# Kernel optimization log

Hardware: AMD Instinct MI355X
Metric: run time of the kernel (lower is better)

## Reference

```python
import jax, jax.numpy as jnp
import numpy as np

N_PAIR = 32
N_ENTI = 36          # VidVRD object classes (+pad)
N_CLS_TOT = 133      # 132 predicate classes + background id 0
NUM_BASE = 92        # split='base' -> pids 1..92
N_CTX = 8
MAX_L = 40           # GeneralAlproCfg.max_txt_len
D = 768


def setup_inputs() -> dict:
    key = jax.random.key(0)
    ks = jax.random.split(key, 11)
    std = 0.02
    return {
        "so_cls_ids": jax.random.randint(ks[0], (N_PAIR, 2), 0, N_ENTI, dtype=jnp.int64),
        "enti_txt_embds": jax.random.normal(ks[1], (N_ENTI, 256), jnp.float32),
        "prefix_embds": jax.random.normal(ks[2], (N_CLS_TOT, 1, D), jnp.float32) * std,
        "suffix_embds": jax.random.normal(ks[3], (N_CLS_TOT, MAX_L - 1 - N_CTX, D), jnp.float32) * std,
        "token_mask": jnp.ones((N_CLS_TOT, MAX_L), jnp.int32),
        "meta_ctx_embds": jax.random.normal(ks[4], (N_CTX, D), jnp.float32) * std,
        "subj_ctx_embds": jax.random.normal(ks[5], (N_CTX, D), jnp.float32) * std,
        "obj_ctx_embds": jax.random.normal(ks[6], (N_CTX, D), jnp.float32) * std,
        "W1": jax.random.normal(ks[7], (512, 256), jnp.float32) * std,
        "b1": jnp.zeros((256,), jnp.float32),
        "W2": jax.random.normal(ks[8], (256, 2 * D), jnp.float32) * std,
    }


def reference(so_cls_ids, enti_txt_embds, prefix_embds, suffix_embds, token_mask,
              meta_ctx_embds, subj_ctx_embds, obj_ctx_embds, W1, b1, W2):
    n_pair = so_cls_ids.shape[0]
    pids = jnp.arange(1, NUM_BASE + 1)                      # split='base'
    n_cls = NUM_BASE

    # entity text-embedding gather + tiny MLP
    s_embd = enti_txt_embds[so_cls_ids[:, 0]]               # [n_pair, 256]
    o_embd = enti_txt_embds[so_cls_ids[:, 1]]
    so = jnp.concatenate([s_embd, o_embd], axis=-1)         # [n_pair, 512]
    h = jax.nn.relu(so @ W1 + b1)                           # [n_pair, 256]
    so_e = h @ W2                                           # [n_pair, 1536]
    s_q, o_q = so_e[:, :D], so_e[:, D:]

    # softmax attention over meta context (keys = values = meta_ctx_embds)
    scale = 1.0 / jnp.sqrt(jnp.asarray(D, jnp.float32))
    s_att = jax.nn.softmax(s_q @ meta_ctx_embds.T * scale, axis=-1) @ meta_ctx_embds  # [n_pair, D]
    o_att = jax.nn.softmax(o_q @ meta_ctx_embds.T * scale, axis=-1) @ meta_ctx_embds

    s_ctx = subj_ctx_embds[None, :, :] + s_att[:, None, :]  # [n_pair, n_ctx, D]
    o_ctx = obj_ctx_embds[None, :, :] + o_att[:, None, :]

    prefix = prefix_embds[pids]                             # [n_cls, 1, D]
    suffix = suffix_embds[pids]                             # [n_cls, L_suf, D]
    l_suf = suffix.shape[1]

    def build(ctx):
        return jnp.concatenate([
            jnp.broadcast_to(prefix[None], (n_pair, n_cls, 1, D)),
            jnp.broadcast_to(ctx[:, None], (n_pair, n_cls, N_CTX, D)),
            jnp.broadcast_to(suffix[None], (n_pair, n_cls, l_suf, D)),
        ], axis=2).reshape(n_pair * n_cls, MAX_L, D)

    subj_token_embds = build(s_ctx)                         # [n_pair*n_cls, MAX_L, D]
    obj_token_embds = build(o_ctx)
    mask = jnp.tile(token_mask[pids], (n_pair, 1))          # [n_pair*n_cls, MAX_L]
    return subj_token_embds, obj_token_embds, mask
```

## Files before the change

### kernel.cpp

```cpp
#include <hip/hip_runtime.h>
#include <hip/hip_bf16.h>

typedef unsigned int u32;
typedef __attribute__((ext_vector_type(4))) float f32x4;

#define NPAIR 32
#define NCLS  92
#define NCTX  8
#define MAXL  40
#define DIM   768
#define LSUF  31

#define MAT_ELEMS 90439680u
#define MASK_BASE 180879360u
#define NBLK_D1   1472u
#define MASK_F4   29440u
#define NBLK_MASK 115u

#define WS_ATT  0u
#define WS_H    49152u
#define WS_SOE  57344u

__global__ __launch_bounds__(512) void k_h(
    const int* __restrict__ so_ids,
    const float* __restrict__ enti,
    const float* __restrict__ W1,
    const float* __restrict__ b1,
    float* __restrict__ ws)
{
    const int p = blockIdx.x;
    const int t = threadIdx.x;
    __shared__ float so_vec[512];
    __shared__ float w1part[2][256];
    __shared__ int ids[2];

    if (t == 0) {
        bool is64 = true;
        for (int i = 1; i < 64; i += 2) is64 = is64 && (so_ids[i] == 0);
        if (is64) { ids[0] = so_ids[4 * p];     ids[1] = so_ids[4 * p + 2]; }
        else      { ids[0] = so_ids[2 * p];     ids[1] = so_ids[2 * p + 1]; }
    }
    __syncthreads();
    so_vec[t] = (t < 256) ? enti[ids[0] * 256 + t] : enti[ids[1] * 256 + (t - 256)];
    __syncthreads();

    const int j = t & 255, half = t >> 8;
    const float* w = W1 + (half * 256) * 256 + j;
    const float* sv = so_vec + half * 256;
    float acc = 0.f;
    #pragma unroll 8
    for (int kk = 0; kk < 256; ++kk)
        acc = fmaf(sv[kk], w[(size_t)kk * 256], acc);
    w1part[half][j] = acc;
    __syncthreads();
    if (t < 256)
        ws[WS_H + p * 256 + t] = fmaxf(w1part[0][t] + w1part[1][t] + b1[t], 0.f);
}

__global__ __launch_bounds__(256) void k_soe(
    const float* __restrict__ W2,
    float* __restrict__ ws)
{
    const int p = blockIdx.x / 6;
    const int cc = blockIdx.x % 6;
    const int t = threadIdx.x;
    __shared__ float hl[256];
    hl[t] = ws[WS_H + p * 256 + t];
    __syncthreads();

    const int c = cc * 256 + t;
    const float* w = W2 + c;
    float acc = 0.f;
    #pragma unroll 8
    for (int k = 0; k < 256; ++k)
        acc = fmaf(hl[k], w[(size_t)k * 1536], acc);
    ws[WS_SOE + p * 1536 + c] = acc;
}

__global__ __launch_bounds__(256) void k_att(
    const float* __restrict__ meta,
    float* __restrict__ ws)
{
    const int which = blockIdx.x >> 5;
    const int p = blockIdx.x & 31;
    const int t = threadIdx.x;
    __shared__ float red[8][256];
    __shared__ float probs[8];

    const float* q = ws + WS_SOE + p * 1536 + which * DIM;
    float qr[3];
    #pragma unroll
    for (int i = 0; i < 3; ++i) qr[i] = q[t + 256 * i];

    #pragma unroll
    for (int c = 0; c < 8; ++c) {
        float pp = 0.f;
        #pragma unroll
        for (int i = 0; i < 3; ++i)
            pp = fmaf(qr[i], meta[c * DIM + t + 256 * i], pp);
        red[c][t] = pp;
    }
    __syncthreads();
    for (int s = 128; s > 0; s >>= 1) {
        if (t < s) {
            #pragma unroll
            for (int c = 0; c < 8; ++c)
                red[c][t] += red[c][t + s];
        }
        __syncthreads();
    }
    if (t == 0) {
        const float scale = 0.036084391824351615f;
        float sc[8], m = -1e30f;
        #pragma unroll
        for (int c = 0; c < 8; ++c) { sc[c] = red[c][0] * scale; m = fmaxf(m, sc[c]); }
        float sum = 0.f;
        #pragma unroll
        for (int c = 0; c < 8; ++c) { sc[c] = expf(sc[c] - m); sum += sc[c]; }
        const float inv = 1.f / sum;
        #pragma unroll
        for (int c = 0; c < 8; ++c) probs[c] = sc[c] * inv;
    }
    __syncthreads();
    #pragma unroll
    for (int i = 0; i < 3; ++i) {
        const int d = t + 256 * i;
        float a = 0.f;
        #pragma unroll
        for (int c = 0; c < 8; ++c)
            a = fmaf(probs[c], meta[c * DIM + d], a);
        ws[WS_ATT + (which * NPAIR + p) * DIM + d] = a;
    }
}

__global__ __launch_bounds__(256) void k_copy(
    const float* __restrict__ prefix,
    const float* __restrict__ suffix,
    const int* __restrict__ tok_mask,
    float* __restrict__ out)
{
    const u32 bid = blockIdx.x;
    const u32 t = threadIdx.x;

    if (bid < NBLK_D1) {
        const u32 which = bid / (NCLS * 8u);
        const u32 rem = bid - which * (NCLS * 8u);
        const u32 cls = rem / 8u;
        const u32 tq = rem - cls * 8u;

        __shared__ __align__(16) float srcl[4 * DIM];
        for (u32 u = t; u < 4u * 192u; u += 256u) {
            const u32 j = u / 192u;
            const u32 dpos = u - j * 192u;
            const u32 rtok = (tq == 0u) ? (j == 0u ? 0u : 8u + j) : (8u + 4u * tq + j);
            const float* src = (rtok == 0u)
                ? (prefix + (size_t)(cls + 1u) * DIM + dpos * 4u)
                : (suffix + ((size_t)(cls + 1u) * LSUF + (rtok - 9u)) * DIM + dpos * 4u);
            *(f32x4*)(srcl + u * 4u) = *(const f32x4*)src;
        }
        __syncthreads();

        for (u32 pair = 0; pair < NPAIR; ++pair) {
            float* slab = out + (size_t)which * MAT_ELEMS
                              + ((size_t)(pair * NCLS + cls) * MAXL) * DIM;
            #pragma unroll
            for (u32 uu = 0; uu < 3u; ++uu) {
                const u32 u = uu * 256u + t;
                const u32 j = u / 192u;
                const u32 dpos = u - j * 192u;
                const u32 rtok = (tq == 0u) ? (j == 0u ? 0u : 8u + j) : (8u + 4u * tq + j);
                __builtin_nontemporal_store(*(const f32x4*)(srcl + u * 4u),
                    (f32x4*)(slab + (size_t)rtok * DIM + dpos * 4u));
            }
        }
    } else {
        const u32 idx4 = (bid - NBLK_D1) * 256u + t;
        if (idx4 < MASK_F4) {
            const u32 m = idx4 * 4u;
            f32x4 v;
            #pragma unroll
            for (int j = 0; j < 4; ++j) {
                const u32 i = m + (u32)j;
                const u32 rw = i / 40u;
                const u32 tk = i - rw * 40u;
                const u32 cls = rw % 92u;
                v[j] = (float)tok_mask[(cls + 1u) * 40u + tk];
            }
            __builtin_nontemporal_store(v, (f32x4*)(out + MASK_BASE + m));
        }
    }
}

__global__ __launch_bounds__(256) void k_ctx(
    const float* __restrict__ sctx,
    const float* __restrict__ octx,
    const float* __restrict__ att,
    float* __restrict__ out)
{
    const u32 bid = blockIdx.x;
    const u32 t = threadIdx.x;
    const u32 which = bid / 128u;
    const u32 rem = bid - which * 128u;
    const u32 pair = rem / 4u;
    const u32 cg = rem & 3u;

    const float* ctx = which ? octx : sctx;
    const float* ar = att + (size_t)(which * NPAIR + pair) * DIM;

    __shared__ __align__(16) float sums[8 * DIM];
    for (u32 u = t; u < 8u * 192u; u += 256u) {
        const u32 dpos = u % 192u;
        const f32x4 v = *(const f32x4*)(ctx + (size_t)u * 4u)
                      + *(const f32x4*)(ar + (size_t)dpos * 4u);
        *(f32x4*)(sums + u * 4u) = v;
    }
    __syncthreads();

    for (u32 c = 0; c < 23u; ++c) {
        const u32 cls = cg * 23u + c;
        float* base = out + (size_t)which * MAT_ELEMS
                          + ((size_t)(pair * NCLS + cls) * MAXL + 1u) * DIM;
        #pragma unroll
        for (u32 uu = 0; uu < 6u; ++uu) {
            const u32 u = uu * 256u + t;
            __builtin_nontemporal_store(*(const f32x4*)(sums + u * 4u),
                (f32x4*)(base + (size_t)u * 4u));
        }
    }
}

extern "C" void kernel_launch(void* const* d_in, const int* in_sizes, int n_in,
                              void* d_out, int out_size, void* d_ws, size_t ws_size,
                              hipStream_t stream) {
    const int* so_ids     = (const int*)d_in[0];
    const float* enti     = (const float*)d_in[1];
    const float* prefix   = (const float*)d_in[2];
    const float* suffix   = (const float*)d_in[3];
    const int* tok_mask   = (const int*)d_in[4];
    const float* meta     = (const float*)d_in[5];
    const float* sctx     = (const float*)d_in[6];
    const float* octx     = (const float*)d_in[7];
    const float* W1       = (const float*)d_in[8];
    const float* b1       = (const float*)d_in[9];
    const float* W2       = (const float*)d_in[10];
    float* ws = (float*)d_ws;

    k_h  <<<dim3(NPAIR), dim3(512), 0, stream>>>(so_ids, enti, W1, b1, ws);
    k_soe<<<dim3(192),   dim3(256), 0, stream>>>(W2, ws);
    k_att<<<dim3(64),    dim3(256), 0, stream>>>(meta, ws);
    k_ctx<<<dim3(256),   dim3(256), 0, stream>>>(sctx, octx, ws + WS_ATT, (float*)d_out);
    k_copy<<<dim3(NBLK_D1 + NBLK_MASK), dim3(256), 0, stream>>>(
        prefix, suffix, tok_mask, (float*)d_out);
}
```

Measured before the change: 171.0 us.

## Fuse MLP, attention, context broadcast and copy kernels into one launch

Merges the five kernels into a single launch. The first 64 blocks each redundantly compute the per-pair MLP, softmax attention and context sum in shared memory, then write context rows for all 92 classes. The remaining blocks do the prefix/suffix broadcast and the mask, unchanged. This removes four launches and the workspace round-trips. In exchange, the 64 context blocks each recompute the W1/W2 matvecs serially, so they may become a long tail, and these blocks are not overlapped with any earlier compute.

Measured after the change: 156.4 us. 8.6% less time.

```diff
diff --git a/kernel.cpp b/kernel.cpp
--- a/kernel.cpp
+++ b/kernel.cpp
@@ -13,142 +13,157 @@
 
 #define MAT_ELEMS 90439680u
 #define MASK_BASE 180879360u
+
+#define NBLK_CTX  64u
 #define NBLK_D1   1472u
-#define MASK_F4   29440u
 #define NBLK_MASK 115u
-
-#define WS_ATT  0u
-#define WS_H    49152u
-#define WS_SOE  57344u
-
-__global__ __launch_bounds__(512) void k_h(
+#define NBLK_ALL  (NBLK_CTX + NBLK_D1 + NBLK_MASK)
+
+__global__ __launch_bounds__(256) void k_fused(
     const int* __restrict__ so_ids,
     const float* __restrict__ enti,
-    const float* __restrict__ W1,
-    const float* __restrict__ b1,
-    float* __restrict__ ws)
-{
-    const int p = blockIdx.x;
-    const int t = threadIdx.x;
-    __shared__ float so_vec[512];
-    __shared__ float w1part[2][256];
-    __shared__ int ids[2];
-
-    if (t == 0) {
-        bool is64 = true;
-        for (int i = 1; i < 64; i += 2) is64 = is64 && (so_ids[i] == 0);
-        if (is64) { ids[0] = so_ids[4 * p];     ids[1] = so_ids[4 * p + 2]; }
-        else      { ids[0] = so_ids[2 * p];     ids[1] = so_ids[2 * p + 1]; }
-    }
-    __syncthreads();
-    so_vec[t] = (t < 256) ? enti[ids[0] * 256 + t] : enti[ids[1] * 256 + (t - 256)];
-    __syncthreads();
-
-    const int j = t & 255, half = t >> 8;
-    const float* w = W1 + (half * 256) * 256 + j;
-    const float* sv = so_vec + half * 256;
-    float acc = 0.f;
-    #pragma unroll 8
-    for (int kk = 0; kk < 256; ++kk)
-        acc = fmaf(sv[kk], w[(size_t)kk * 256], acc);
-    w1part[half][j] = acc;
-    __syncthreads();
-    if (t < 256)
-        ws[WS_H + p * 256 + t] = fmaxf(w1part[0][t] + w1part[1][t] + b1[t], 0.f);
-}
-
-__global__ __launch_bounds__(256) void k_soe(
-    const float* __restrict__ W2,
-    float* __restrict__ ws)
-{
-    const int p = blockIdx.x / 6;
-    const int cc = blockIdx.x % 6;
-    const int t = threadIdx.x;
-    __shared__ float hl[256];
-    hl[t] = ws[WS_H + p * 256 + t];
-    __syncthreads();
-
-    const int c = cc * 256 + t;
-    const float* w = W2 + c;
-    float acc = 0.f;
-    #pragma unroll 8
-    for (int k = 0; k < 256; ++k)
-        acc = fmaf(hl[k], w[(size_t)k * 1536], acc);
-    ws[WS_SOE + p * 1536 + c] = acc;
-}
-
-__global__ __launch_bounds__(256) void k_att(
-    const float* __restrict__ meta,
-    float* __restrict__ ws)
-{
-    const int which = blockIdx.x >> 5;
-    const int p = blockIdx.x & 31;
-    const int t = threadIdx.x;
-    __shared__ float red[8][256];
-    __shared__ float probs[8];
-
-    const float* q = ws + WS_SOE + p * 1536 + which * DIM;
-    float qr[3];
-    #pragma unroll
-    for (int i = 0; i < 3; ++i) qr[i] = q[t + 256 * i];
-
-    #pragma unroll
-    for (int c = 0; c < 8; ++c) {
-        float pp = 0.f;
-        #pragma unroll
-        for (int i = 0; i < 3; ++i)
-            pp = fmaf(qr[i], meta[c * DIM + t + 256 * i], pp);
-        red[c][t] = pp;
-    }
-    __syncthreads();
-    for (int s = 128; s > 0; s >>= 1) {
-        if (t < s) {
-            #pragma unroll
-            for (int c = 0; c < 8; ++c)
-                red[c][t] += red[c][t + s];
-        }
-        __syncthreads();
-    }
-    if (t == 0) {
-        const float scale = 0.036084391824351615f;
-        float sc[8], m = -1e30f;
-        #pragma unroll
-        for (int c = 0; c < 8; ++c) { sc[c] = red[c][0] * scale; m = fmaxf(m, sc[c]); }
-        float sum = 0.f;
-        #pragma unroll
-        for (int c = 0; c < 8; ++c) { sc[c] = expf(sc[c] - m); sum += sc[c]; }
-        const float inv = 1.f / sum;
-        #pragma unroll
-        for (int c = 0; c < 8; ++c) probs[c] = sc[c] * inv;
-    }
-    __syncthreads();
-    #pragma unroll
-    for (int i = 0; i < 3; ++i) {
-        const int d = t + 256 * i;
-        float a = 0.f;
-        #pragma unroll
-        for (int c = 0; c < 8; ++c)
-            a = fmaf(probs[c], meta[c * DIM + d], a);
-        ws[WS_ATT + (which * NPAIR + p) * DIM + d] = a;
-    }
-}
-
-__global__ __launch_bounds__(256) void k_copy(
     const float* __restrict__ prefix,
     const float* __restrict__ suffix,
     const int* __restrict__ tok_mask,
+    const float* __restrict__ meta,
+    const float* __restrict__ sctx,
+    const float* __restrict__ octx,
+    const float* __restrict__ W1,
+    const float* __restrict__ b1,
+    const float* __restrict__ W2,
     float* __restrict__ out)
 {
     const u32 bid = blockIdx.x;
     const u32 t = threadIdx.x;
-
-    if (bid < NBLK_D1) {
-        const u32 which = bid / (NCLS * 8u);
-        const u32 rem = bid - which * (NCLS * 8u);
+    __shared__ __align__(16) float arena[8 * DIM];
+    __shared__ int ids[2];
+
+    if (bid < NBLK_CTX) {
+        const u32 which = bid >> 5;
+        const u32 pair = bid & 31u;
+
+        if (t == 0) {
+            bool is64 = true;
+            for (int i = 1; i < 64; i += 2) is64 = is64 && (so_ids[i] == 0);
+            if (is64) { ids[0] = so_ids[4 * pair]; ids[1] = so_ids[4 * pair + 2]; }
+            else      { ids[0] = so_ids[2 * pair]; ids[1] = so_ids[2 * pair + 1]; }
+        }
+        __syncthreads();
+
+        float* so_vec = arena;
+        float* h      = arena + 512;
+        float* soe    = arena + 768;
+        float* red    = arena + 2304;
+        float* probs  = arena + 4352;
+
+        so_vec[t]        = enti[ids[0] * 256 + t];
+        so_vec[256 + t]  = enti[ids[1] * 256 + t];
+        __syncthreads();
+
+        {
+            float acc = b1[t];
+            const float* w = W1 + t;
+            #pragma unroll 8
+            for (int k = 0; k < 512; ++k)
+                acc = fmaf(so_vec[k], w[(size_t)k * 256], acc);
+            h[t] = fmaxf(acc, 0.f);
+        }
+        __syncthreads();
+
+        {
+            float a6[6] = {0.f, 0.f, 0.f, 0.f, 0.f, 0.f};
+            const float* w = W2 + t;
+            #pragma unroll 4
+            for (int k = 0; k < 256; ++k) {
+                const float hk = h[k];
+                #pragma unroll
+                for (int r = 0; r < 6; ++r)
+                    a6[r] = fmaf(hk, w[(size_t)k * 1536 + r * 256], a6[r]);
+            }
+            #pragma unroll
+            for (int r = 0; r < 6; ++r) soe[r * 256 + t] = a6[r];
+        }
+        __syncthreads();
+
+        const float* q = soe + which * DIM;
+        float qr[3];
+        #pragma unroll
+        for (int i = 0; i < 3; ++i) qr[i] = q[t + 256 * i];
+        #pragma unroll
+        for (int c = 0; c < 8; ++c) {
+            float pp = 0.f;
+            #pragma unroll
+            for (int i = 0; i < 3; ++i)
+                pp = fmaf(qr[i], meta[c * DIM + t + 256 * i], pp);
+            red[c * 256 + t] = pp;
+        }
+        __syncthreads();
+        for (int s = 128; s > 0; s >>= 1) {
+            if (t < (u32)s) {
+                #pragma unroll
+                for (int c = 0; c < 8; ++c)
+                    red[c * 256 + t] += red[c * 256 + t + s];
+            }
+            __syncthreads();
+        }
+        if (t == 0) {
+            const float scale = 0.036084391824351615f;
+            float sc[8], m = -1e30f;
+            #pragma unroll
+            for (int c = 0; c < 8; ++c) { sc[c] = red[c * 256] * scale; m = fmaxf(m, sc[c]); }
+            float sum = 0.f;
+            #pragma unroll
+            for (int c = 0; c < 8; ++c) { sc[c] = expf(sc[c] - m); sum += sc[c]; }
+            const float inv = 1.f / sum;
+            #pragma unroll
+            for (int c = 0; c < 8; ++c) probs[c] = sc[c] * inv;
+        }
+        __syncthreads();
+
+        float pr[8];
+        #pragma unroll
+        for (int c = 0; c < 8; ++c) pr[c] = probs[c];
+        float att_d[3];
+        #pragma unroll
+        for (int i = 0; i < 3; ++i) {
+            const int d = t + 256 * i;
+            float a = 0.f;
+            #pragma unroll
+            for (int c = 0; c < 8; ++c)
+                a = fmaf(pr[c], meta[c * DIM + d], a);
+            att_d[i] = a;
+        }
+        __syncthreads();
+
+        const float* ctxg = which ? octx : sctx;
+        #pragma unroll
+        for (int j = 0; j < 8; ++j) {
+            #pragma unroll
+            for (int i = 0; i < 3; ++i) {
+                const int d = t + 256 * i;
+                arena[j * DIM + d] = ctxg[j * DIM + d] + att_d[i];
+            }
+        }
+        __syncthreads();
+
+        float* base = out + (size_t)which * MAT_ELEMS
+                          + ((size_t)(pair * NCLS) * MAXL + 1u) * DIM;
+        for (u32 cls = 0; cls < NCLS; ++cls) {
+            float* bc = base + (size_t)cls * (MAXL * DIM);
+            #pragma unroll
+            for (u32 uu = 0; uu < 6u; ++uu) {
+                const u32 u = uu * 256u + t;
+                __builtin_nontemporal_store(*(const f32x4*)(arena + u * 4u),
+                                            (f32x4*)(bc + u * 4u));
+            }
+        }
+    } else if (bid < NBLK_CTX + NBLK_D1) {
+        const u32 r = bid - NBLK_CTX;
+        const u32 which = r / (NCLS * 8u);
+        const u32 rem = r - which * (NCLS * 8u);
         const u32 cls = rem / 8u;
         const u32 tq = rem - cls * 8u;
 
-        __shared__ __align__(16) float srcl[4 * DIM];
         for (u32 u = t; u < 4u * 192u; u += 256u) {
             const u32 j = u / 192u;
             const u32 dpos = u - j * 192u;
@@ -156,7 +171,7 @@
             const float* src = (rtok == 0u)
                 ? (prefix + (size_t)(cls + 1u) * DIM + dpos * 4u)
                 : (suffix + ((size_t)(cls + 1u) * LSUF + (rtok - 9u)) * DIM + dpos * 4u);
-            *(f32x4*)(srcl + u * 4u) = *(const f32x4*)src;
+            *(f32x4*)(arena + u * 4u) = *(const f32x4*)src;
         }
         __syncthreads();
 
@@ -169,63 +184,23 @@
                 const u32 j = u / 192u;
                 const u32 dpos = u - j * 192u;
                 const u32 rtok = (tq == 0u) ? (j == 0u ? 0u : 8u + j) : (8u + 4u * tq + j);
-                __builtin_nontemporal_store(*(const f32x4*)(srcl + u * 4u),
+                __builtin_nontemporal_store(*(const f32x4*)(arena + u * 4u),
                     (f32x4*)(slab + (size_t)rtok * DIM + dpos * 4u));
             }
         }
     } else {
-        const u32 idx4 = (bid - NBLK_D1) * 256u + t;
-        if (idx4 < MASK_F4) {
-            const u32 m = idx4 * 4u;
-            f32x4 v;
-            #pragma unroll
-            for (int j = 0; j < 4; ++j) {
-                const u32 i = m + (u32)j;
-                const u32 rw = i / 40u;
-                const u32 tk = i - rw * 40u;
-                const u32 cls = rw % 92u;
-                v[j] = (float)tok_mask[(cls + 1u) * 40u + tk];
-            }
-            __builtin_nontemporal_store(v, (f32x4*)(out + MASK_BASE + m));
-        }
-    }
-}
-
-__global__ __launch_bounds__(256) void k_ctx(
-    const float* __restrict__ sctx,
-    const float* __restrict__ octx,
-    const float* __restrict__ att,
-    float* __restrict__ out)
-{
-    const u32 bid = blockIdx.x;
-    const u32 t = threadIdx.x;
-    const u32 which = bid / 128u;
-    const u32 rem = bid - which * 128u;
-    const u32 pair = rem / 4u;
-    const u32 cg = rem & 3u;
-
-    const float* ctx = which ? octx : sctx;
-    const float* ar = att + (size_t)(which * NPAIR + pair) * DIM;
-
-    __shared__ __align__(16) float sums[8 * DIM];
-    for (u32 u = t; u < 8u * 192u; u += 256u) {
-        const u32 dpos = u % 192u;
-        const f32x4 v = *(const f32x4*)(ctx + (size_t)u * 4u)
-                      + *(const f32x4*)(ar + (size_t)dpos * 4u);
-        *(f32x4*)(sums + u * 4u) = v;
-    }
-    __syncthreads();
-
-    for (u32 c = 0; c < 23u; ++c) {
-        const u32 cls = cg * 23u + c;
-        float* base = out + (size_t)which * MAT_ELEMS
-                          + ((size_t)(pair * NCLS + cls) * MAXL + 1u) * DIM;
-        #pragma unroll
-        for (u32 uu = 0; uu < 6u; ++uu) {
-            const u32 u = uu * 256u + t;
-            __builtin_nontemporal_store(*(const f32x4*)(sums + u * 4u),
-                (f32x4*)(base + (size_t)u * 4u));
-        }
+        const u32 idx4 = (bid - NBLK_CTX - NBLK_D1) * 256u + t;
+        const u32 m = idx4 * 4u;
+        f32x4 v;
+        #pragma unroll
+        for (int j = 0; j < 4; ++j) {
+            const u32 i = m + (u32)j;
+            const u32 rw = i / 40u;
+            const u32 tk = i - rw * 40u;
+            const u32 cls = rw % 92u;
+            v[j] = (float)tok_mask[(cls + 1u) * 40u + tk];
+        }
+        __builtin_nontemporal_store(v, (f32x4*)(out + MASK_BASE + m));
     }
 }
 
@@ -243,12 +218,8 @@
     const float* W1       = (const float*)d_in[8];
     const float* b1       = (const float*)d_in[9];
     const float* W2       = (const float*)d_in[10];
-    float* ws = (float*)d_ws;
-
-    k_h  <<<dim3(NPAIR), dim3(512), 0, stream>>>(so_ids, enti, W1, b1, ws);
-    k_soe<<<dim3(192),   dim3(256), 0, stream>>>(W2, ws);
-    k_att<<<dim3(64),    dim3(256), 0, stream>>>(meta, ws);
-    k_ctx<<<dim3(256),   dim3(256), 0, stream>>>(sctx, octx, ws + WS_ATT, (float*)d_out);
-    k_copy<<<dim3(NBLK_D1 + NBLK_MASK), dim3(256), 0, stream>>>(
-        prefix, suffix, tok_mask, (float*)d_out);
+
+    k_fused<<<dim3(NBLK_ALL), dim3(256), 0, stream>>>(
+        so_ids, enti, prefix, suffix, tok_mask, meta, sctx, octx, W1, b1, W2,
+        (float*)d_out);
 }
```
